# Performance work log

Hardware: AMD Instinct MI355X
Metric: run time of the kernel (lower is better)

## Reference

```python
import jax, jax.numpy as jnp
import numpy as np

NEG_INF = -1e9


def setup_inputs() -> dict:
    key = jax.random.key(0)
    k1, k2, k3 = jax.random.split(key, 3)
    B, C, Q, D = 64, 1024, 128, 128
    context = jax.random.normal(k1, (B, C, D), dtype=jnp.float32)
    query = jax.random.normal(k2, (B, Q, D), dtype=jnp.float32)
    W = jax.random.normal(k3, (3 * D, 1), dtype=jnp.float32)
    query_mask = jnp.ones((B, Q), dtype=jnp.float32)
    return {"context": context, "query": query, "W": W, "query_mask": query_mask}


def reference(context, query, W, query_mask):
    # Dense(1) over concat([c, q, c*q]) decomposes as c.w_c + q.w_q + (c*w_s).q
    D = context.shape[-1]
    w = W[:, 0]
    w_c, w_q, w_s = w[:D], w[D:2 * D], w[2 * D:]
    c_term = jnp.einsum('bcd,d->bc', context, w_c)          # [B,C]
    q_term = jnp.einsum('bqd,d->bq', query, w_q)            # [B,Q]
    s_term = jnp.einsum('bcd,bqd->bcq', context * w_s, query)  # [B,C,Q]
    S = c_term[:, :, None] + q_term[:, None, :] + s_term    # [B,C,Q]
    S = S + (1.0 - query_mask)[:, None, :] * NEG_INF
    c2q_scores = jax.nn.softmax(S, axis=2)                  # [B,C,Q]
    c2q = jnp.einsum('bcq,bqd->bcd', c2q_scores, query)     # [B,C,D]
    q2c_scores = jax.nn.softmax(jnp.max(S, axis=2), axis=1)  # [B,C]
    q2c = jnp.einsum('bc,bcd->bd', q2c_scores, context)     # [B,D]
    q2c = q2c[:, None, :]                                   # broadcast over C
    out = jnp.concatenate([context, c2q, context * c2q, context * q2c], axis=-1)
    return out
```

## Files before the change

### kernel.cpp

```cpp
#include <hip/hip_runtime.h>

#define NEGINF -1000000000.0f

typedef __attribute__((ext_vector_type(4))) float f32x4;
typedef _Float16 half8 __attribute__((ext_vector_type(8)));
typedef _Float16 half4 __attribute__((ext_vector_type(4)));

constexpr int Bn = 64, Cn = 1024, Qn = 128, Dn = 128;
constexpr int QSTR = 136;
constexpr int CSTR = 132;

__global__ __launch_bounds__(512) void k0_kernel(
    const float* __restrict__ qry, const float* __restrict__ W,
    const float* __restrict__ mask,
    _Float16* __restrict__ qh, _Float16* __restrict__ qT2p, float* __restrict__ qts_g)
{
    __shared__ float wq[128];
    __shared__ _Float16 qs[128][132];
    const int b = blockIdx.x, t = threadIdx.x;
    if (t < 128) wq[t] = W[128 + t];
    __syncthreads();

    {
        int q = t >> 2, h = t & 3;
        const float* qr = qry + ((size_t)b * Qn + q) * Dn + h * 32;
        float acc = 0.f;
        for (int j = 0; j < 32; j += 4) {
            f32x4 v = *(const f32x4*)(qr + j);
            int d = h * 32 + j;
            acc += v.x * wq[d] + v.y * wq[d + 1] + v.z * wq[d + 2] + v.w * wq[d + 3];
            half4 hv;
            hv[0] = (_Float16)v.x; hv[1] = (_Float16)v.y;
            hv[2] = (_Float16)v.z; hv[3] = (_Float16)v.w;
            *(half4*)&qh[((size_t)b * Qn + q) * Dn + d] = hv;
            *(half4*)&qs[q][d] = hv;
        }
        acc += __shfl_xor(acc, 1);
        acc += __shfl_xor(acc, 2);
        if (h == 0) qts_g[b * Qn + q] = acc + (1.0f - mask[b * Qn + q]) * NEGINF;
    }
    __syncthreads();
    {
        int d = t >> 2, h = t & 3;
#pragma unroll
        for (int blk = 0; blk < 4; ++blk) {
            int i0 = h * 32 + blk * 8;
            half8 w;
#pragma unroll
            for (int j = 0; j < 8; ++j) {
                int i = i0 + j;
                int q = (i & ~31) | (((i >> 2) & 1) << 4) | (((i >> 3) & 3) << 2) | (i & 3);
                w[j] = qs[q][d];
            }
            *(half8*)&qT2p[((size_t)b * Dn + d) * Qn + i0] = w;
        }
    }
}

__global__ __launch_bounds__(512, 4) void k1_kernel(
    const float* __restrict__ ctx, const _Float16* __restrict__ qh,
    const _Float16* __restrict__ qT2p, const float* __restrict__ qts_g,
    const float* __restrict__ W,
    float* __restrict__ out, float* __restrict__ ws_part, float* __restrict__ ws_ms)
{
    __shared__ char smem[72256];
    _Float16* qrow = (_Float16*)smem;
    _Float16* rows = (_Float16*)smem;
    float* wfull = (float*)(smem + 69632);
    float* qts   = (float*)(smem + 70656);
    float* mloc  = (float*)(smem + 71168);
    float* wv    = (float*)(smem + 71680);
    float* red   = (float*)(smem + 72192);
    _Float16* qT2 = (_Float16*)(smem + 34816);
    float* cq    = (float*)smem;
    float* partf = (float*)smem;

    const int b = blockIdx.y, cg = blockIdx.x, c0 = cg * 128;
    const int t = threadIdx.x;
    const float* ctxB = ctx + (size_t)b * Cn * Dn;

    {
        int r = t >> 1, h = t & 1;
        const _Float16* src = (r < 128)
            ? qh   + ((size_t)b * Qn + r) * Dn + h * 64
            : qT2p + ((size_t)b * Dn + (r - 128)) * Qn + h * 64;
        _Float16* dst = rows + r * QSTR + h * 64;
#pragma unroll
        for (int s = 0; s < 8; ++s)
            *(half8*)(dst + s * 8) = *(const half8*)(src + s * 8);
    }
    if (t < 128) wfull[t] = W[t];
    else if (t < 256) wfull[t] = W[256 + (t - 128)];
    if (t < 128) qts[t] = qts_g[b * Qn + t];
    __syncthreads();

    const int wave = t >> 6, lane = t & 63, g = lane >> 4, l15 = lane & 15;
    const int cw = wave * 16;
    const int cl = cw + l15;

    f32x4 acc1[8] = {};
    float cterm = 0.f;
#pragma unroll
    for (int kk = 0; kk < 4; ++kk) {
        const int dbase = kk * 32 + g * 8;
        const float* pc = ctxB + (size_t)(c0 + cl) * Dn + dbase;
        f32x4 v0 = *(const f32x4*)pc, v1 = *(const f32x4*)(pc + 4);
        f32x4 s0 = *(const f32x4*)&wfull[128 + dbase], s1 = *(const f32x4*)&wfull[128 + dbase + 4];
        f32x4 c0w = *(const f32x4*)&wfull[dbase], c1w = *(const f32x4*)&wfull[dbase + 4];
        cterm += v0.x * c0w.x + v0.y * c0w.y + v0.z * c0w.z + v0.w * c0w.w
               + v1.x * c1w.x + v1.y * c1w.y + v1.z * c1w.z + v1.w * c1w.w;
        half8 ah;
        ah[0] = (_Float16)(v0.x * s0.x); ah[1] = (_Float16)(v0.y * s0.y);
        ah[2] = (_Float16)(v0.z * s0.z); ah[3] = (_Float16)(v0.w * s0.w);
        ah[4] = (_Float16)(v1.x * s1.x); ah[5] = (_Float16)(v1.y * s1.y);
        ah[6] = (_Float16)(v1.z * s1.z); ah[7] = (_Float16)(v1.w * s1.w);
#pragma unroll
        for (int mt = 0; mt < 8; ++mt) {
            half8 qf = *(const half8*)&qrow[(mt * 16 + l15) * QSTR + dbase];
            acc1[mt] = __builtin_amdgcn_mfma_f32_16x16x32_f16(qf, ah, acc1[mt], 0, 0, 0);
        }
    }
    cterm += __shfl_xor(cterm, 16);
    cterm += __shfl_xor(cterm, 32);

#pragma unroll
    for (int mt = 0; mt < 8; ++mt)
#pragma unroll
        for (int r = 0; r < 4; ++r) acc1[mt][r] += qts[mt * 16 + g * 4 + r];

    float mx = -3.4e38f;
#pragma unroll
    for (int mt = 0; mt < 8; ++mt)
#pragma unroll
        for (int r = 0; r < 4; ++r) mx = fmaxf(mx, acc1[mt][r]);
    mx = fmaxf(mx, __shfl_xor(mx, 16));
    mx = fmaxf(mx, __shfl_xor(mx, 32));
    float sum = 0.f;
#pragma unroll
    for (int mt = 0; mt < 8; ++mt)
#pragma unroll
        for (int r = 0; r < 4; ++r) {
            float pv = __expf(acc1[mt][r] - mx);
            acc1[mt][r] = pv;
            sum += pv;
        }
    sum += __shfl_xor(sum, 16);
    sum += __shfl_xor(sum, 32);
    if (g == 0) mloc[cl] = mx + cterm;

    half8 pa[4];
#pragma unroll
    for (int kk2 = 0; kk2 < 4; ++kk2)
#pragma unroll
        for (int j = 0; j < 8; ++j)
            pa[kk2][j] = (_Float16)acc1[2 * kk2 + (j >> 2)][j & 3];

    float inv[4];
#pragma unroll
    for (int r = 0; r < 4; ++r) inv[r] = 1.0f / __shfl(sum, g * 4 + r);

    f32x4 acc2[8] = {};
#pragma unroll
    for (int kk2 = 0; kk2 < 4; ++kk2)
#pragma unroll
        for (int ntD = 0; ntD < 8; ++ntD) {
            half8 qb = *(const half8*)&qT2[(ntD * 16 + l15) * QSTR + kk2 * 32 + 8 * g];
            acc2[ntD] = __builtin_amdgcn_mfma_f32_16x16x32_f16(pa[kk2], qb, acc2[ntD], 0, 0, 0);
        }
    __syncthreads();

#pragma unroll
    for (int r = 0; r < 4; ++r) {
        int c = cw + g * 4 + r;
        float is = inv[r];
#pragma unroll
        for (int ntD = 0; ntD < 8; ++ntD)
            cq[c * CSTR + ntD * 16 + l15] = acc2[ntD][r] * is;
    }
    __syncthreads();

    const int grp = t >> 5, d4 = (t & 31) * 4;
#pragma unroll
    for (int step = 0; step < 8; ++step) {
        int c = grp + step * 16;
        f32x4 q = *(const f32x4*)&cq[c * CSTR + d4];
        f32x4 cv = *(const f32x4*)(ctxB + (size_t)(c0 + c) * Dn + d4);
        float* orow = out + ((size_t)(b * Cn + c0 + c)) * 512;
        __builtin_nontemporal_store(q, (f32x4*)(orow + 128 + d4));
        f32x4 pr;
        pr.x = cv.x * q.x; pr.y = cv.y * q.y; pr.z = cv.z * q.z; pr.w = cv.w * q.w;
        __builtin_nontemporal_store(pr, (f32x4*)(orow + 256 + d4));
    }

    float vm = mloc[t & 127];
    float m = vm;
#pragma unroll
    for (int off = 1; off < 64; off <<= 1) m = fmaxf(m, __shfl_xor(m, off));
    if (lane == 0) red[wave] = m;
    __syncthreads();
    float Mloc = red[0];
#pragma unroll
    for (int i = 1; i < 8; ++i) Mloc = fmaxf(Mloc, red[i]);
    float e = __expf(vm - Mloc);
    if (t < 128) wv[t] = e;
    float s = e;
#pragma unroll
    for (int off = 1; off < 64; off <<= 1) s += __shfl_xor(s, off);
    if (lane == 0) red[8 + wave] = s;
    __syncthreads();
    float Sloc = red[8] + red[9];

    {
        const float* cb = ctxB + (size_t)(c0 + grp * 8) * Dn;
        f32x4 a = {};
#pragma unroll
        for (int i = 0; i < 8; ++i) {
            f32x4 cv = *(const f32x4*)(cb + (size_t)i * Dn + d4);
            float w = wv[grp * 8 + i];
            a.x += w * cv.x; a.y += w * cv.y; a.z += w * cv.z; a.w += w * cv.w;
        }
        *(f32x4*)&partf[grp * 128 + d4] = a;
    }
    __syncthreads();
    if (t < 128) {
        float s2 = 0.f;
#pragma unroll
        for (int g2 = 0; g2 < 16; ++g2) s2 += partf[g2 * 128 + t];
        ws_part[((size_t)(b * 8 + cg)) * 128 + t] = s2;
    }
    if (t == 0) {
        ws_ms[(b * 8 + cg) * 2 + 0] = Mloc;
        ws_ms[(b * 8 + cg) * 2 + 1] = Sloc;
    }
}

__global__ __launch_bounds__(256) void k3_kernel(
    const float* __restrict__ ctx, const float* __restrict__ ws_part,
    const float* __restrict__ ws_ms, float* __restrict__ out)
{
    __shared__ float q2cs[128];
    const int ct = blockIdx.x, b = blockIdx.y, t = threadIdx.x;
    if (t < 128) {
        const float* ms = ws_ms + b * 16;
        float Mg = -3.4e38f;
#pragma unroll
        for (int i = 0; i < 8; ++i) Mg = fmaxf(Mg, ms[2 * i]);
        float num = 0.f, den = 0.f;
#pragma unroll
        for (int i = 0; i < 8; ++i) {
            float e = __expf(ms[2 * i] - Mg);
            num += e * ws_part[((size_t)(b * 8 + i)) * 128 + t];
            den += e * ms[2 * i + 1];
        }
        q2cs[t] = num / den;
    }
    __syncthreads();
    const float* cb = ctx + ((size_t)b * Cn + ct * 128) * Dn;
    float* ob = out + ((size_t)(b * Cn) + ct * 128) * 512;
    for (int step = 0; step < 16; ++step) {
        int c = (t >> 5) + step * 8, d4 = (t & 31) * 4;
        f32x4 v = *(const f32x4*)(cb + (size_t)c * Dn + d4);
        f32x4 q = *(const f32x4*)&q2cs[d4];
        __builtin_nontemporal_store(v, (f32x4*)(ob + (size_t)c * 512 + d4));
        f32x4 w;
        w.x = v.x * q.x; w.y = v.y * q.y; w.z = v.z * q.z; w.w = v.w * q.w;
        __builtin_nontemporal_store(w, (f32x4*)(ob + (size_t)c * 512 + 384 + d4));
    }
}

extern "C" void kernel_launch(void* const* d_in, const int* in_sizes, int n_in,
                              void* d_out, int out_size, void* d_ws, size_t ws_size,
                              hipStream_t stream) {
    const float* ctx  = (const float*)d_in[0];
    const float* qry  = (const float*)d_in[1];
    const float* W    = (const float*)d_in[2];
    const float* mask = (const float*)d_in[3];
    float* out = (float*)d_out;

    float* ws_part  = (float*)d_ws;
    float* ws_ms    = ws_part + (size_t)Bn * 8 * 128;
    float* qts_g    = ws_ms + (size_t)Bn * 16;
    _Float16* qh    = (_Float16*)(qts_g + (size_t)Bn * Qn);
    _Float16* qT2p  = qh + (size_t)Bn * Qn * Dn;

    k0_kernel<<<dim3(Bn), 512, 0, stream>>>(qry, W, mask, qh, qT2p, qts_g);
    k1_kernel<<<dim3(8, Bn), 512, 0, stream>>>(ctx, qh, qT2p, qts_g, W, out, ws_part, ws_ms);
    k3_kernel<<<dim3(8, Bn), 256, 0, stream>>>(ctx, ws_part, ws_ms, out);
}
```

Measured before the change: 51.46 us.

## Pre-swizzle query MFMA fragments globally and drop LDS staging in attention kernel

The query precompute kernel now writes Q and its transposed operand directly in per-lane MFMA fragment order, so the main kernel reads fragments from global memory with coalesced loads instead of staging 70KB in LDS. The main kernel shrinks to 256 threads and 64 context rows per block with a doubled grid, does the q2c softmax partial reduction per wave with shuffles, and writes c2q outputs straight from MFMA registers, which removes most barriers. The context copy to the output moves from the final kernel into the main kernel. In exchange the c2q stores become scattered scalar writes, nontemporal hints are dropped, and the final kernel merges twice as many partials.

```diff
diff --git a/kernel.cpp b/kernel.cpp
--- a/kernel.cpp
+++ b/kernel.cpp
@@ -3,107 +3,103 @@
 #define NEGINF -1000000000.0f
 
 typedef __attribute__((ext_vector_type(4))) float f32x4;
+typedef __attribute__((ext_vector_type(2))) float f32x2;
 typedef _Float16 half8 __attribute__((ext_vector_type(8)));
 typedef _Float16 half4 __attribute__((ext_vector_type(4)));
 
 constexpr int Bn = 64, Cn = 1024, Qn = 128, Dn = 128;
-constexpr int QSTR = 136;
-constexpr int CSTR = 132;
-
-__global__ __launch_bounds__(512) void k0_kernel(
+
+__global__ __launch_bounds__(256) void k0_kernel(
     const float* __restrict__ qry, const float* __restrict__ W,
     const float* __restrict__ mask,
-    _Float16* __restrict__ qh, _Float16* __restrict__ qT2p, float* __restrict__ qts_g)
+    _Float16* __restrict__ qA, _Float16* __restrict__ qB, float* __restrict__ qts_g)
 {
     __shared__ float wq[128];
-    __shared__ _Float16 qs[128][132];
+    __shared__ _Float16 qs[128][136];
     const int b = blockIdx.x, t = threadIdx.x;
     if (t < 128) wq[t] = W[128 + t];
     __syncthreads();
 
     {
-        int q = t >> 2, h = t & 3;
-        const float* qr = qry + ((size_t)b * Qn + q) * Dn + h * 32;
+        int q = t >> 1, h = t & 1;
+        const float* qr = qry + ((size_t)b * Qn + q) * Dn + h * 64;
         float acc = 0.f;
-        for (int j = 0; j < 32; j += 4) {
+        for (int j = 0; j < 64; j += 4) {
             f32x4 v = *(const f32x4*)(qr + j);
-            int d = h * 32 + j;
+            int d = h * 64 + j;
             acc += v.x * wq[d] + v.y * wq[d + 1] + v.z * wq[d + 2] + v.w * wq[d + 3];
             half4 hv;
             hv[0] = (_Float16)v.x; hv[1] = (_Float16)v.y;
             hv[2] = (_Float16)v.z; hv[3] = (_Float16)v.w;
-            *(half4*)&qh[((size_t)b * Qn + q) * Dn + d] = hv;
             *(half4*)&qs[q][d] = hv;
         }
         acc += __shfl_xor(acc, 1);
-        acc += __shfl_xor(acc, 2);
         if (h == 0) qts_g[b * Qn + q] = acc + (1.0f - mask[b * Qn + q]) * NEGINF;
     }
     __syncthreads();
+
     {
-        int d = t >> 2, h = t & 3;
-#pragma unroll
-        for (int blk = 0; blk < 4; ++blk) {
-            int i0 = h * 32 + blk * 8;
+        int fm = t >> 3;
+        int l0 = (t & 7) * 8;
+        int kk = fm >> 3, mt = fm & 7;
+        _Float16* dst = qA + ((size_t)b * 32 + fm) * 512;
+#pragma unroll
+        for (int l = l0; l < l0 + 8; ++l) {
+            int q = mt * 16 + (l & 15), d = kk * 32 + (l >> 4) * 8;
+            *(half8*)&dst[l * 8] = *(const half8*)&qs[q][d];
+        }
+    }
+    {
+        int fm = t >> 3;
+        int l0 = (t & 7) * 8;
+        int kk2 = fm >> 3, ntD = fm & 7;
+        _Float16* dst = qB + ((size_t)b * 32 + fm) * 512;
+#pragma unroll
+        for (int l = l0; l < l0 + 8; ++l) {
+            int d = ntD * 16 + (l & 15);
             half8 w;
 #pragma unroll
             for (int j = 0; j < 8; ++j) {
-                int i = i0 + j;
+                int i = kk2 * 32 + (l >> 4) * 8 + j;
                 int q = (i & ~31) | (((i >> 2) & 1) << 4) | (((i >> 3) & 3) << 2) | (i & 3);
                 w[j] = qs[q][d];
             }
-            *(half8*)&qT2p[((size_t)b * Dn + d) * Qn + i0] = w;
-        }
-    }
-}
-
-__global__ __launch_bounds__(512, 4) void k1_kernel(
-    const float* __restrict__ ctx, const _Float16* __restrict__ qh,
-    const _Float16* __restrict__ qT2p, const float* __restrict__ qts_g,
+            *(half8*)&dst[l * 8] = w;
+        }
+    }
+}
+
+__global__ __launch_bounds__(256, 4) void k1_kernel(
+    const float* __restrict__ ctx, const _Float16* __restrict__ qA,
+    const _Float16* __restrict__ qB, const float* __restrict__ qts_g,
     const float* __restrict__ W,
     float* __restrict__ out, float* __restrict__ ws_part, float* __restrict__ ws_ms)
 {
-    __shared__ char smem[72256];
-    _Float16* qrow = (_Float16*)smem;
-    _Float16* rows = (_Float16*)smem;
-    float* wfull = (float*)(smem + 69632);
-    float* qts   = (float*)(smem + 70656);
-    float* mloc  = (float*)(smem + 71168);
-    float* wv    = (float*)(smem + 71680);
-    float* red   = (float*)(smem + 72192);
-    _Float16* qT2 = (_Float16*)(smem + 34816);
-    float* cq    = (float*)smem;
-    float* partf = (float*)smem;
-
-    const int b = blockIdx.y, cg = blockIdx.x, c0 = cg * 128;
+    __shared__ float wfull[256];
+    __shared__ float qts[128];
+    __shared__ float mw_s[4], sw_s[4];
+    __shared__ float partf[4][128];
+
+    const int b = blockIdx.y, cg = blockIdx.x;
     const int t = threadIdx.x;
+    const int wave = t >> 6, lane = t & 63, g = lane >> 4, l15 = lane & 15;
+    const int c0 = cg * 64 + wave * 16;
     const float* ctxB = ctx + (size_t)b * Cn * Dn;
 
-    {
-        int r = t >> 1, h = t & 1;
-        const _Float16* src = (r < 128)
-            ? qh   + ((size_t)b * Qn + r) * Dn + h * 64
-            : qT2p + ((size_t)b * Dn + (r - 128)) * Qn + h * 64;
-        _Float16* dst = rows + r * QSTR + h * 64;
-#pragma unroll
-        for (int s = 0; s < 8; ++s)
-            *(half8*)(dst + s * 8) = *(const half8*)(src + s * 8);
-    }
     if (t < 128) wfull[t] = W[t];
-    else if (t < 256) wfull[t] = W[256 + (t - 128)];
+    else if (t < 256) wfull[t] = W[256 + t - 128];
     if (t < 128) qts[t] = qts_g[b * Qn + t];
     __syncthreads();
 
-    const int wave = t >> 6, lane = t & 63, g = lane >> 4, l15 = lane & 15;
-    const int cw = wave * 16;
-    const int cl = cw + l15;
+    const _Float16* qAb = qA + (size_t)b * 32 * 512;
+    const _Float16* qBb = qB + (size_t)b * 32 * 512;
 
     f32x4 acc1[8] = {};
     float cterm = 0.f;
 #pragma unroll
     for (int kk = 0; kk < 4; ++kk) {
         const int dbase = kk * 32 + g * 8;
-        const float* pc = ctxB + (size_t)(c0 + cl) * Dn + dbase;
+        const float* pc = ctxB + (size_t)(c0 + l15) * Dn + dbase;
         f32x4 v0 = *(const f32x4*)pc, v1 = *(const f32x4*)(pc + 4);
         f32x4 s0 = *(const f32x4*)&wfull[128 + dbase], s1 = *(const f32x4*)&wfull[128 + dbase + 4];
         f32x4 c0w = *(const f32x4*)&wfull[dbase], c1w = *(const f32x4*)&wfull[dbase + 4];
@@ -116,7 +112,7 @@
         ah[6] = (_Float16)(v1.z * s1.z); ah[7] = (_Float16)(v1.w * s1.w);
 #pragma unroll
         for (int mt = 0; mt < 8; ++mt) {
-            half8 qf = *(const half8*)&qrow[(mt * 16 + l15) * QSTR + dbase];
+            half8 qf = *(const half8*)&qAb[(size_t)(kk * 8 + mt) * 512 + lane * 8];
             acc1[mt] = __builtin_amdgcn_mfma_f32_16x16x32_f16(qf, ah, acc1[mt], 0, 0, 0);
         }
     }
@@ -146,7 +142,6 @@
         }
     sum += __shfl_xor(sum, 16);
     sum += __shfl_xor(sum, 32);
-    if (g == 0) mloc[cl] = mx + cterm;
 
     half8 pa[4];
 #pragma unroll
@@ -159,78 +154,67 @@
 #pragma unroll
     for (int r = 0; r < 4; ++r) inv[r] = 1.0f / __shfl(sum, g * 4 + r);
 
+    float mcol = mx + cterm;
+    float Mw = mcol;
+#pragma unroll
+    for (int off = 1; off < 16; off <<= 1) Mw = fmaxf(Mw, __shfl_xor(Mw, off));
+    float ecol = __expf(mcol - Mw);
+    float Sw = ecol;
+#pragma unroll
+    for (int off = 1; off < 16; off <<= 1) Sw += __shfl_xor(Sw, off);
+
+    f32x2 part = {};
+    const int dl = lane * 2;
+#pragma unroll
+    for (int i = 0; i < 16; ++i) {
+        int c = c0 + i;
+        f32x2 cv = *(const f32x2*)(ctxB + (size_t)c * Dn + dl);
+        float e = __shfl(ecol, i);
+        part.x += e * cv.x; part.y += e * cv.y;
+        *(f32x2*)(out + ((size_t)(b * Cn + c)) * 512 + dl) = cv;
+    }
+
     f32x4 acc2[8] = {};
 #pragma unroll
     for (int kk2 = 0; kk2 < 4; ++kk2)
 #pragma unroll
         for (int ntD = 0; ntD < 8; ++ntD) {
-            half8 qb = *(const half8*)&qT2[(ntD * 16 + l15) * QSTR + kk2 * 32 + 8 * g];
+            half8 qb = *(const half8*)&qBb[(size_t)(kk2 * 8 + ntD) * 512 + lane * 8];
             acc2[ntD] = __builtin_amdgcn_mfma_f32_16x16x32_f16(pa[kk2], qb, acc2[ntD], 0, 0, 0);
         }
-    __syncthreads();
 
 #pragma unroll
     for (int r = 0; r < 4; ++r) {
-        int c = cw + g * 4 + r;
+        int c = c0 + g * 4 + r;
         float is = inv[r];
-#pragma unroll
-        for (int ntD = 0; ntD < 8; ++ntD)
-            cq[c * CSTR + ntD * 16 + l15] = acc2[ntD][r] * is;
-    }
-    __syncthreads();
-
-    const int grp = t >> 5, d4 = (t & 31) * 4;
-#pragma unroll
-    for (int step = 0; step < 8; ++step) {
-        int c = grp + step * 16;
-        f32x4 q = *(const f32x4*)&cq[c * CSTR + d4];
-        f32x4 cv = *(const f32x4*)(ctxB + (size_t)(c0 + c) * Dn + d4);
-        float* orow = out + ((size_t)(b * Cn + c0 + c)) * 512;
-        __builtin_nontemporal_store(q, (f32x4*)(orow + 128 + d4));
-        f32x4 pr;
-        pr.x = cv.x * q.x; pr.y = cv.y * q.y; pr.z = cv.z * q.z; pr.w = cv.w * q.w;
-        __builtin_nontemporal_store(pr, (f32x4*)(orow + 256 + d4));
-    }
-
-    float vm = mloc[t & 127];
-    float m = vm;
-#pragma unroll
-    for (int off = 1; off < 64; off <<= 1) m = fmaxf(m, __shfl_xor(m, off));
-    if (lane == 0) red[wave] = m;
-    __syncthreads();
-    float Mloc = red[0];
-#pragma unroll
-    for (int i = 1; i < 8; ++i) Mloc = fmaxf(Mloc, red[i]);
-    float e = __expf(vm - Mloc);
-    if (t < 128) wv[t] = e;
-    float s = e;
-#pragma unroll
-    for (int off = 1; off < 64; off <<= 1) s += __shfl_xor(s, off);
-    if (lane == 0) red[8 + wave] = s;
-    __syncthreads();
-    float Sloc = red[8] + red[9];
-
-    {
-        const float* cb = ctxB + (size_t)(c0 + grp * 8) * Dn;
-        f32x4 a = {};
-#pragma unroll
-        for (int i = 0; i < 8; ++i) {
-            f32x4 cv = *(const f32x4*)(cb + (size_t)i * Dn + d4);
-            float w = wv[grp * 8 + i];
-            a.x += w * cv.x; a.y += w * cv.y; a.z += w * cv.z; a.w += w * cv.w;
-        }
-        *(f32x4*)&partf[grp * 128 + d4] = a;
-    }
+        const float* crow = ctxB + (size_t)c * Dn;
+        float* orow = out + ((size_t)(b * Cn + c)) * 512;
+#pragma unroll
+        for (int ntD = 0; ntD < 8; ++ntD) {
+            int d = ntD * 16 + l15;
+            float c2 = acc2[ntD][r] * is;
+            orow[128 + d] = c2;
+            orow[256 + d] = crow[d] * c2;
+        }
+    }
+
+    *(f32x2*)&partf[wave][dl] = part;
+    if (lane == 0) { mw_s[wave] = Mw; sw_s[wave] = Sw; }
     __syncthreads();
     if (t < 128) {
-        float s2 = 0.f;
-#pragma unroll
-        for (int g2 = 0; g2 < 16; ++g2) s2 += partf[g2 * 128 + t];
-        ws_part[((size_t)(b * 8 + cg)) * 128 + t] = s2;
-    }
-    if (t == 0) {
-        ws_ms[(b * 8 + cg) * 2 + 0] = Mloc;
-        ws_ms[(b * 8 + cg) * 2 + 1] = Sloc;
+        float M = fmaxf(fmaxf(mw_s[0], mw_s[1]), fmaxf(mw_s[2], mw_s[3]));
+        float p = 0.f, S = 0.f;
+#pragma unroll
+        for (int w = 0; w < 4; ++w) {
+            float e = __expf(mw_s[w] - M);
+            p += e * partf[w][t];
+            S += e * sw_s[w];
+        }
+        ws_part[((size_t)(b * 16 + cg)) * 128 + t] = p;
+        if (t == 0) {
+            ws_ms[(b * 16 + cg) * 2 + 0] = M;
+            ws_ms[(b * 16 + cg) * 2 + 1] = S;
+        }
     }
 }
 
@@ -241,15 +225,15 @@
     __shared__ float q2cs[128];
     const int ct = blockIdx.x, b = blockIdx.y, t = threadIdx.x;
     if (t < 128) {
-        const float* ms = ws_ms + b * 16;
+        const float* ms = ws_ms + b * 32;
         float Mg = -3.4e38f;
 #pragma unroll
-        for (int i = 0; i < 8; ++i) Mg = fmaxf(Mg, ms[2 * i]);
+        for (int i = 0; i < 16; ++i) Mg = fmaxf(Mg, ms[2 * i]);
         float num = 0.f, den = 0.f;
 #pragma unroll
-        for (int i = 0; i < 8; ++i) {
+        for (int i = 0; i < 16; ++i) {
             float e = __expf(ms[2 * i] - Mg);
-            num += e * ws_part[((size_t)(b * 8 + i)) * 128 + t];
+            num += e * ws_part[((size_t)(b * 16 + i)) * 128 + t];
             den += e * ms[2 * i + 1];
         }
         q2cs[t] = num / den;
@@ -261,10 +245,9 @@
         int c = (t >> 5) + step * 8, d4 = (t & 31) * 4;
         f32x4 v = *(const f32x4*)(cb + (size_t)c * Dn + d4);
         f32x4 q = *(const f32x4*)&q2cs[d4];
-        __builtin_nontemporal_store(v, (f32x4*)(ob + (size_t)c * 512 + d4));
         f32x4 w;
         w.x = v.x * q.x; w.y = v.y * q.y; w.z = v.z * q.z; w.w = v.w * q.w;
-        __builtin_nontemporal_store(w, (f32x4*)(ob + (size_t)c * 512 + 384 + d4));
+        *(f32x4*)(ob + (size_t)c * 512 + 384 + d4) = w;
     }
 }
 
@@ -277,13 +260,13 @@
     const float* mask = (const float*)d_in[3];
     float* out = (float*)d_out;
 
-    float* ws_part  = (float*)d_ws;
-    float* ws_ms    = ws_part + (size_t)Bn * 8 * 128;
-    float* qts_g    = ws_ms + (size_t)Bn * 16;
-    _Float16* qh    = (_Float16*)(qts_g + (size_t)Bn * Qn);
-    _Float16* qT2p  = qh + (size_t)Bn * Qn * Dn;
-
-    k0_kernel<<<dim3(Bn), 512, 0, stream>>>(qry, W, mask, qh, qT2p, qts_g);
-    k1_kernel<<<dim3(8, Bn), 512, 0, stream>>>(ctx, qh, qT2p, qts_g, W, out, ws_part, ws_ms);
+    float* ws_part = (float*)d_ws;
+    float* ws_ms   = ws_part + (size_t)Bn * 16 * 128;
+    float* qts_g   = ws_ms + (size_t)Bn * 32;
+    _Float16* qA   = (_Float16*)(qts_g + (size_t)Bn * Qn);
+    _Float16* qB   = qA + (size_t)Bn * 32 * 512;
+
+    k0_kernel<<<dim3(Bn), 256, 0, stream>>>(qry, W, mask, qA, qB, qts_g);
+    k1_kernel<<<dim3(16, Bn), 256, 0, stream>>>(ctx, qA, qB, qts_g, W, out, ws_part, ws_ms);
     k3_kernel<<<dim3(8, Bn), 256, 0, stream>>>(ctx, ws_part, ws_ms, out);
 }
```

Measured after the change: 68.80 us. +33.7%, slower.
